# Kernel tuning notes

Measured on AMD Instinct MI355X. Metric: run time of the kernel, lower is better.

## Reference

```python
import jax, jax.numpy as jnp
import numpy as np

B, D, N = 2048, 512, 100000


def setup_inputs() -> dict:
    key = jax.random.key(0)
    k1, k2, k3 = jax.random.split(key, 3)
    queries = jax.random.normal(k1, (B, D), dtype=jnp.float32)
    X = jax.random.normal(k2, (N, D), dtype=jnp.float32)
    Y = jax.random.randint(k3, (N,), 0, 2, dtype=jnp.int64)
    return {"queries": queries, "X": X, "Y": Y, "K": 5}


def reference(queries, X, Y, K):
    # Pairwise squared Euclidean distance: ||q||^2 - 2 q.X^T + ||x||^2.
    # Use negative distance so lax.top_k returns nearest neighbors.
    q2 = jnp.sum(queries * queries, axis=1, keepdims=True)        # [B, 1]
    x2 = jnp.sum(X * X, axis=1)                                   # [N]
    neg_dist = 2.0 * (queries @ X.T) - q2 - x2[None, :]           # [B, N]
    _, idx = jax.lax.top_k(neg_dist, K)                           # [B, K]
    # Gather neighbor labels and count votes (fraction of class-1 neighbors).
    neighbor_labels = Y[idx].astype(jnp.float32)                  # [B, K]
    votes = jnp.mean(neighbor_labels, axis=1)                     # [B]
    # tf.pad(tf.expand_dims(votes, 1), [[0,0],[0,1]]) -> [B, 2]
    return jnp.pad(votes[:, None], ((0, 0), (0, 1)))
```

## Files before the change

### kernel.cpp

```cpp
#include <hip/hip_runtime.h>
#include <math.h>

typedef unsigned int   u32;
typedef unsigned short u16;
typedef short short8 __attribute__((ext_vector_type(8)));
typedef float f32x4  __attribute__((ext_vector_type(4)));

constexpr int B    = 2048;
constexpr int D    = 512;
constexpr int N    = 100000;
constexpr int KTOP = 5;
constexpr int NK   = 16;

constexpr int NPART    = 32;
constexpr int CHUNK    = 3136;
constexpr int PGPART   = CHUNK / 16;
constexpr int NPTS_PAD = NPART * CHUNK;
constexpr int NPG      = NPTS_PAD / 16;

__device__ __forceinline__ u16 f2bf(float f) {
    u32 u = __float_as_uint(f);
    return (u16)((u + 0x7fffu + ((u >> 16) & 1u)) >> 16);
}

__device__ __forceinline__ void gld_lds16(const void* g, void* l) {
    __builtin_amdgcn_global_load_lds((const __attribute__((address_space(1))) u32*)g,
                                     (__attribute__((address_space(3))) u32*)l, 16, 0, 0);
}

__device__ __forceinline__ void ins5(float (&s)[KTOP], int (&x)[KTOP], float v, int p) {
    if (v > s[KTOP - 1]) {
        s[KTOP - 1] = v; x[KTOP - 1] = p;
#pragma unroll
        for (int k = KTOP - 1; k > 0; --k) {
            if (s[k] > s[k - 1]) {
                float tf = s[k]; s[k] = s[k - 1]; s[k - 1] = tf;
                int   tg = x[k]; x[k] = x[k - 1]; x[k - 1] = tg;
            }
        }
    }
}

__device__ __forceinline__ void merge_xor(float (&s)[KTOP], int (&x)[KTOP], int mask) {
    float bs[KTOP], as[KTOP]; int bx[KTOP], ax[KTOP];
#pragma unroll
    for (int k = 0; k < KTOP; ++k) {
        bs[k] = __shfl_xor(s[k], mask); bx[k] = __shfl_xor(x[k], mask);
        as[k] = s[k]; ax[k] = x[k];
    }
#pragma unroll
    for (int k = 0; k < KTOP; ++k) {
        bool ta = (as[0] > bs[0]) || ((as[0] == bs[0]) && (ax[0] < bx[0]));
        s[k] = ta ? as[0] : bs[0];
        x[k] = ta ? ax[0] : bx[0];
#pragma unroll
        for (int m = 0; m < KTOP - 1; ++m) {
            as[m] = ta ? as[m + 1] : as[m];     ax[m] = ta ? ax[m + 1] : ax[m];
            bs[m] = ta ? bs[m]     : bs[m + 1]; bx[m] = ta ? bx[m]     : bx[m + 1];
        }
        as[KTOP - 1] = ta ? -INFINITY : as[KTOP - 1];
        bs[KTOP - 1] = ta ? bs[KTOP - 1] : -INFINITY;
    }
}

__global__ void prep_q(const float* __restrict__ Q, u16* __restrict__ Qbf) {
    int tid  = blockIdx.x * 256 + threadIdx.x;
    int q    = tid >> 6;
    int koct = tid & 63;
    const float4* src = (const float4*)(Q + (size_t)q * D + koct * 8);
    float4 a = src[0], b = src[1];
    u32 p0 = (u32)f2bf(a.x) | ((u32)f2bf(a.y) << 16);
    u32 p1 = (u32)f2bf(a.z) | ((u32)f2bf(a.w) << 16);
    u32 p2 = (u32)f2bf(b.x) | ((u32)f2bf(b.y) << 16);
    u32 p3 = (u32)f2bf(b.z) | ((u32)f2bf(b.w) << 16);
    int frag = (q >> 4) * NK + (koct >> 2);
    int lane = (q & 15) + 16 * (koct & 3);
    *(uint4*)(Qbf + (size_t)frag * 512 + lane * 8) = make_uint4(p0, p1, p2, p3);
}

__global__ void prep_x2(const float* __restrict__ X, u16* __restrict__ Xbf,
                        float* __restrict__ x2) {
    __shared__ float psum[4][16];
    const int t = threadIdx.x, lane = t & 63, wave = t >> 6;
    const int pg    = blockIdx.x;
    const int point = pg * 16 + (lane & 15);
    float ssum = 0.f;
#pragma unroll
    for (int u = 0; u < 4; ++u) {
        int k0i = wave * 4 + u;
        int k   = k0i * 32 + ((lane >> 4) << 3);
        uint4 o = make_uint4(0u, 0u, 0u, 0u);
        if (point < N) {
            const float4* src = (const float4*)(X + (size_t)point * D + k);
            float4 a = src[0], b = src[1];
            ssum = fmaf(a.x, a.x, ssum); ssum = fmaf(a.y, a.y, ssum);
            ssum = fmaf(a.z, a.z, ssum); ssum = fmaf(a.w, a.w, ssum);
            ssum = fmaf(b.x, b.x, ssum); ssum = fmaf(b.y, b.y, ssum);
            ssum = fmaf(b.z, b.z, ssum); ssum = fmaf(b.w, b.w, ssum);
            o.x = (u32)f2bf(a.x) | ((u32)f2bf(a.y) << 16);
            o.y = (u32)f2bf(a.z) | ((u32)f2bf(a.w) << 16);
            o.z = (u32)f2bf(b.x) | ((u32)f2bf(b.y) << 16);
            o.w = (u32)f2bf(b.z) | ((u32)f2bf(b.w) << 16);
        }
        *(uint4*)(Xbf + ((size_t)pg * 16 + k0i) * 512 + lane * 8) = o;
    }
    ssum += __shfl_xor(ssum, 16);
    ssum += __shfl_xor(ssum, 32);
    if (lane < 16) psum[wave][lane] = ssum;
    __syncthreads();
    if (t < 16) {
        float s = psum[0][t] + psum[1][t] + psum[2][t] + psum[3][t];
        x2[pg * 16 + t] = (pg * 16 + t < N) ? s : INFINITY;
    }
}

__global__ void x2_kernel(const float* __restrict__ X, float* __restrict__ x2, int total) {
    int lane = threadIdx.x & 63;
    int wid  = (int)((blockIdx.x * blockDim.x + threadIdx.x) >> 6);
    if (wid >= total) return;
    if (wid >= N) { if (lane == 0) x2[wid] = INFINITY; return; }
    const float* row = X + (size_t)wid * D;
    float s = 0.f;
    for (int c = lane; c < D; c += 64) { float v = row[c]; s = fmaf(v, v, s); }
#pragma unroll
    for (int off = 32; off > 0; off >>= 1) s += __shfl_down(s, off);
    if (lane == 0) x2[wid] = s;
}

__launch_bounds__(256, 2)
__global__ void knn_qreg(const u16* __restrict__ Xbf, const u16* __restrict__ Qbf,
                         const float* __restrict__ x2g,
                         float* __restrict__ cand_s, int* __restrict__ cand_i) {
    __shared__ __attribute__((aligned(16))) u16 Afr[2][16 * 512];
    const int t    = threadIdx.x;
    const int lane = t & 63;
    const int wave = t >> 6;
    const int quad = lane >> 4;
    const int col  = lane & 15;
    const int qb   = blockIdx.x;
    const int part = blockIdx.y;
    const int pg0    = part * PGPART;
    const int pstart = part * CHUNK;

    short8 bq[2][16];
#pragma unroll
    for (int j = 0; j < 2; ++j) {
        int qg = qb * 8 + wave * 2 + j;
#pragma unroll
        for (int k0i = 0; k0i < 16; ++k0i)
            bq[j][k0i] = *(const short8*)(Qbf + ((size_t)qg * 16 + k0i) * 512 + lane * 8);
    }

    float ss[2][KTOP]; int si[2][KTOP];
#pragma unroll
    for (int j = 0; j < 2; ++j)
#pragma unroll
        for (int k = 0; k < KTOP; ++k) { ss[j][k] = -INFINITY; si[j][k] = 0x7fffffff; }

    auto issue = [&](int pgi, int bsel) {
        const u16* src = Xbf + ((size_t)(pg0 + pgi) * 16 + wave * 4) * 512 + lane * 8;
        u16* dst = Afr[bsel] + (wave * 4) * 512;
#pragma unroll
        for (int f = 0; f < 4; ++f)
            gld_lds16(src + f * 512, dst + f * 512);
    };

    issue(0, 0);
    for (int pgi = 0; pgi < PGPART; ++pgi) {
        const int bsel = pgi & 1;
        __syncthreads();
        if (pgi + 1 < PGPART) issue(pgi + 1, bsel ^ 1);
        const int P = pstart + pgi * 16;
        float4 xx = *(const float4*)(x2g + P + quad * 4);

        f32x4 acc0 = (f32x4)0.f, acc1 = (f32x4)0.f;
#pragma unroll
        for (int k0i = 0; k0i < 16; ++k0i) {
            short8 af = *(const short8*)&Afr[bsel][k0i * 512 + lane * 8];
            acc0 = __builtin_amdgcn_mfma_f32_16x16x32_bf16(af, bq[0][k0i], acc0, 0, 0, 0);
            acc1 = __builtin_amdgcn_mfma_f32_16x16x32_bf16(af, bq[1][k0i], acc1, 0, 0, 0);
        }
        const int gbase = P + quad * 4;
        {
            float s0 = fmaf(2.f, acc0[0], -xx.x);
            float s1 = fmaf(2.f, acc0[1], -xx.y);
            float s2 = fmaf(2.f, acc0[2], -xx.z);
            float s3 = fmaf(2.f, acc0[3], -xx.w);
            float mx = fmaxf(fmaxf(s0, s1), fmaxf(s2, s3));
            if (mx > ss[0][KTOP - 1]) {
                ins5(ss[0], si[0], s0, gbase + 0);
                ins5(ss[0], si[0], s1, gbase + 1);
                ins5(ss[0], si[0], s2, gbase + 2);
                ins5(ss[0], si[0], s3, gbase + 3);
            }
        }
        {
            float s0 = fmaf(2.f, acc1[0], -xx.x);
            float s1 = fmaf(2.f, acc1[1], -xx.y);
            float s2 = fmaf(2.f, acc1[2], -xx.z);
            float s3 = fmaf(2.f, acc1[3], -xx.w);
            float mx = fmaxf(fmaxf(s0, s1), fmaxf(s2, s3));
            if (mx > ss[1][KTOP - 1]) {
                ins5(ss[1], si[1], s0, gbase + 0);
                ins5(ss[1], si[1], s1, gbase + 1);
                ins5(ss[1], si[1], s2, gbase + 2);
                ins5(ss[1], si[1], s3, gbase + 3);
            }
        }
    }

#pragma unroll
    for (int j = 0; j < 2; ++j) { merge_xor(ss[j], si[j], 16); merge_xor(ss[j], si[j], 32); }
    if (quad == 0) {
#pragma unroll
        for (int j = 0; j < 2; ++j) {
            int q = qb * 128 + wave * 32 + j * 16 + col;
            size_t base = ((size_t)q * NPART + part) * KTOP;
#pragma unroll
            for (int k = 0; k < KTOP; ++k) { cand_s[base + k] = ss[j][k]; cand_i[base + k] = si[j][k]; }
        }
    }
}

__launch_bounds__(256)
__global__ void knn_conv(const float* __restrict__ X, const u16* __restrict__ Qbf,
                         const float* __restrict__ x2g,
                         float* __restrict__ cand_s, int* __restrict__ cand_i) {
    __shared__ __attribute__((aligned(16))) u16 Bfr[16 * 512];
    __shared__ __attribute__((aligned(16))) u16 Afr[4 * 512];
    __shared__ float x2s[64];
    const int t = threadIdx.x, lane = t & 63, wave = t >> 6;
    const int quad = lane >> 4, col = lane & 15;
    const int qb = blockIdx.x, part = blockIdx.y;
    const int pstart = part * 782;
    const int pend   = min(pstart + 782, N);

    float ss[4][KTOP]; int si[4][KTOP];
#pragma unroll
    for (int j = 0; j < 4; ++j)
#pragma unroll
        for (int k = 0; k < KTOP; ++k) { ss[j][k] = -INFINITY; si[j][k] = 0x7fffffff; }

    const int nsub = (pend - pstart + 63) / 64;
    for (int sbi = 0; sbi < nsub; ++sbi) {
        const int sb = pstart + sbi * 64;
        __syncthreads();
        if (t < 64) x2s[t] = (sb + t < pend) ? x2g[sb + t] : INFINITY;
        f32x4 acc[4][4];
#pragma unroll
        for (int i = 0; i < 4; ++i)
#pragma unroll
            for (int j = 0; j < 4; ++j) acc[i][j] = (f32x4)0.f;
        for (int k0i = 0; k0i < NK; ++k0i) {
            const int k0 = k0i * 32;
            __syncthreads();
            {
                int prow = sb + wave * 16 + col;
                if (prow >= pend) prow = pend - 1;
                const float4* src = (const float4*)(X + (size_t)prow * D + k0 + quad * 8);
                float4 a = src[0], b = src[1];
                u32 p0 = (u32)f2bf(a.x) | ((u32)f2bf(a.y) << 16);
                u32 p1 = (u32)f2bf(a.z) | ((u32)f2bf(a.w) << 16);
                u32 p2 = (u32)f2bf(b.x) | ((u32)f2bf(b.y) << 16);
                u32 p3 = (u32)f2bf(b.z) | ((u32)f2bf(b.w) << 16);
                *(uint4*)(Afr + wave * 512 + lane * 8) = make_uint4(p0, p1, p2, p3);
            }
#pragma unroll
            for (int j = 0; j < 4; ++j) {
                int qgrp = qb * 16 + wave * 4 + j;
                gld_lds16(Qbf + ((size_t)qgrp * NK + k0i) * 512 + lane * 8,
                          (void*)(Bfr + (wave * 4 + j) * 512));
            }
            __syncthreads();
            short8 af[4], bqf[4];
#pragma unroll
            for (int i = 0; i < 4; ++i) af[i] = *(const short8*)(Afr + i * 512 + lane * 8);
#pragma unroll
            for (int j = 0; j < 4; ++j) bqf[j] = *(const short8*)(Bfr + (wave * 4 + j) * 512 + lane * 8);
#pragma unroll
            for (int i = 0; i < 4; ++i)
#pragma unroll
                for (int j = 0; j < 4; ++j)
                    acc[i][j] = __builtin_amdgcn_mfma_f32_16x16x32_bf16(af[i], bqf[j], acc[i][j], 0, 0, 0);
        }
#pragma unroll
        for (int i = 0; i < 4; ++i) {
            int pb = 16 * i + quad * 4;
#pragma unroll
            for (int j = 0; j < 4; ++j)
#pragma unroll
                for (int r = 0; r < 4; ++r)
                    ins5(ss[j], si[j], 2.f * acc[i][j][r] - x2s[pb + r], sb + pb + r);
        }
    }
#pragma unroll
    for (int j = 0; j < 4; ++j) { merge_xor(ss[j], si[j], 16); merge_xor(ss[j], si[j], 32); }
    if (quad == 0) {
#pragma unroll
        for (int j = 0; j < 4; ++j) {
            int qg = qb * 256 + wave * 64 + j * 16 + col;
            size_t base = ((size_t)qg * 128 + part) * KTOP;
#pragma unroll
            for (int k = 0; k < KTOP; ++k) { cand_s[base + k] = ss[j][k]; cand_i[base + k] = si[j][k]; }
        }
    }
}

__launch_bounds__(256)
__global__ void finalize(const float* __restrict__ Q, const float* __restrict__ X,
                         const float* __restrict__ x2g, const int* __restrict__ Y,
                         const float* __restrict__ cand_s, const int* __restrict__ cand_i,
                         float* __restrict__ out, int npart) {
    __shared__ float scs[4][96];
    __shared__ int   sis[4][96];
    const int t = threadIdx.x, lane = t & 63, w = t >> 6;
    const int q = blockIdx.x * 4 + w;
    const int perlane = npart * KTOP / 16;

    if (lane < 16) {
        float ls[KTOP]; int li[KTOP];
#pragma unroll
        for (int k = 0; k < KTOP; ++k) { ls[k] = -INFINITY; li[k] = 0x7fffffff; }
        const float* cs = cand_s + (size_t)q * npart * KTOP + lane * perlane;
        const int*   ci = cand_i + (size_t)q * npart * KTOP + lane * perlane;
        for (int c = 0; c < perlane; ++c) {
            float s = cs[c]; int p = ci[c];
            if (s > ls[KTOP - 1] || (s == ls[KTOP - 1] && p < li[KTOP - 1])) {
                ls[KTOP - 1] = s; li[KTOP - 1] = p;
#pragma unroll
                for (int k = KTOP - 1; k > 0; --k) {
                    bool up = (ls[k] > ls[k - 1]) || (ls[k] == ls[k - 1] && li[k] < li[k - 1]);
                    if (up) {
                        float tf = ls[k]; ls[k] = ls[k - 1]; ls[k - 1] = tf;
                        int   tg = li[k]; li[k] = li[k - 1]; li[k - 1] = tg;
                    }
                }
            }
        }
#pragma unroll
        for (int k = 0; k < KTOP; ++k) { scs[w][lane * KTOP + k] = ls[k]; sis[w][lane * KTOP + k] = li[k]; }
    }
    __syncthreads();
    if (lane == 0) {
        float bs[16]; int bx[16];
#pragma unroll
        for (int m = 0; m < 16; ++m) { bs[m] = -INFINITY; bx[m] = 0x7fffffff; }
        for (int c = 0; c < 80; ++c) {
            float s = scs[w][c]; int p = sis[w][c];
            if (s > bs[15] || (s == bs[15] && p < bx[15])) {
                bs[15] = s; bx[15] = p;
#pragma unroll
                for (int m = 15; m > 0; --m) {
                    bool up = (bs[m] > bs[m - 1]) || (bs[m] == bs[m - 1] && bx[m] < bx[m - 1]);
                    if (up) {
                        float tf = bs[m]; bs[m] = bs[m - 1]; bs[m - 1] = tf;
                        int   tg = bx[m]; bx[m] = bx[m - 1]; bx[m - 1] = tg;
                    }
                }
            }
        }
#pragma unroll
        for (int m = 0; m < 16; ++m) sis[w][80 + m] = bx[m];
    }
    __syncthreads();
    const int c = lane & 15, seg = lane >> 4;
    int idx = sis[w][80 + c];
    const float4* xr = (const float4*)(X + (size_t)idx * D);
    const float4* qr = (const float4*)(Q + (size_t)q * D);
    float d = 0.f;
    for (int u = seg * 32; u < seg * 32 + 32; ++u) {
        float4 a = qr[u], b = xr[u];
        d = fmaf(a.x, b.x, d); d = fmaf(a.y, b.y, d);
        d = fmaf(a.z, b.z, d); d = fmaf(a.w, b.w, d);
    }
    d += __shfl_xor(d, 16);
    d += __shfl_xor(d, 32);
    float sc = 2.f * d - x2g[idx];
    if (seg == 0) scs[w][80 + c] = sc;
    __syncthreads();
    if (lane == 0) {
        float bs[KTOP]; int bx[KTOP];
#pragma unroll
        for (int k = 0; k < KTOP; ++k) { bs[k] = -INFINITY; bx[k] = 0x7fffffff; }
        for (int c2 = 0; c2 < 16; ++c2) {
            float s = scs[w][80 + c2]; int p = sis[w][80 + c2];
            if (s > bs[KTOP - 1] || (s == bs[KTOP - 1] && p < bx[KTOP - 1])) {
                bs[KTOP - 1] = s; bx[KTOP - 1] = p;
#pragma unroll
                for (int k = KTOP - 1; k > 0; --k) {
                    bool up = (bs[k] > bs[k - 1]) || (bs[k] == bs[k - 1] && bx[k] < bx[k - 1]);
                    if (up) {
                        float tf = bs[k]; bs[k] = bs[k - 1]; bs[k - 1] = tf;
                        int   tg = bx[k]; bx[k] = bx[k - 1]; bx[k - 1] = tg;
                    }
                }
            }
        }
        float sum = 0.f;
#pragma unroll
        for (int k = 0; k < KTOP; ++k) sum += (float)Y[bx[k]];
        out[2 * q]     = sum * 0.2f;
        out[2 * q + 1] = 0.f;
    }
}

extern "C" void kernel_launch(void* const* d_in, const int* in_sizes, int n_in,
                              void* d_out, int out_size, void* d_ws, size_t ws_size,
                              hipStream_t stream) {
    const float* Qf = (const float*)d_in[0];
    const float* Xf = (const float*)d_in[1];
    const int*   Y  = (const int*)d_in[2];
    float* out = (float*)d_out;
    char* ws = (char*)d_ws;

    constexpr size_t XBF_B  = (size_t)NPG * NK * 1024;
    constexpr size_t QBF_B  = 2097152;
    constexpr size_t X2_B   = (size_t)NPTS_PAD * 4;
    constexpr size_t CAND_B = (size_t)B * NPART * KTOP * 4;
    constexpr size_t NEED   = XBF_B + QBF_B + X2_B + 2 * CAND_B;

    if (ws_size >= NEED) {
        u16*   Xbf    = (u16*)ws;
        u16*   Qbf    = (u16*)(ws + XBF_B);
        float* x2     = (float*)(ws + XBF_B + QBF_B);
        float* cand_s = (float*)(ws + XBF_B + QBF_B + X2_B);
        int*   cand_i = (int*)  (ws + XBF_B + QBF_B + X2_B + CAND_B);
        hipLaunchKernelGGL(prep_q,   dim3(512),           dim3(256), 0, stream, Qf, Qbf);
        hipLaunchKernelGGL(prep_x2,  dim3(NPG),           dim3(256), 0, stream, Xf, Xbf, x2);
        hipLaunchKernelGGL(knn_qreg, dim3(16, NPART),     dim3(256), 0, stream, Xbf, Qbf, x2, cand_s, cand_i);
        hipLaunchKernelGGL(finalize, dim3(B / 4),         dim3(256), 0, stream, Qf, Xf, x2, Y, cand_s, cand_i, out, NPART);
    } else {
        u16*   Qbf    = (u16*)ws;
        float* x2     = (float*)(ws + 2097152);
        float* cand_s = (float*)(ws + 2497152);
        int*   cand_i = (int*)  (ws + 7740032);
        hipLaunchKernelGGL(prep_q,    dim3(512),      dim3(256), 0, stream, Qf, Qbf);
        hipLaunchKernelGGL(x2_kernel, dim3(N / 4),    dim3(256), 0, stream, Xf, x2, N);
        hipLaunchKernelGGL(knn_conv,  dim3(8, 128),   dim3(256), 0, stream, Xf, Qbf, x2, cand_s, cand_i);
        hipLaunchKernelGGL(finalize,  dim3(B / 4),    dim3(256), 0, stream, Qf, Xf, x2, Y, cand_s, cand_i, out, 128);
    }
}
```

Measured before the change: 699.5 us.

## Double partitions, process two point groups per stage, swap grid axes

Raises the number of point partitions from 32 to 64 so the knn grid grows from 512 to 1024 blocks. Each pipeline stage now loads and computes two 16-point groups, giving four independent MFMA chains per step and halving the barrier count. The grid axes are swapped so adjacent blocks share the same query tile, and a compiler barrier keeps the query register loads in place. The costs are twice the LDS per block, more registers for accumulators, and twice as many candidates for finalize to merge.

New measurement: 692.7 us. Within noise of the previous version (-1.0%).

```diff
diff --git a/kernel.cpp b/kernel.cpp
--- a/kernel.cpp
+++ b/kernel.cpp
@@ -12,11 +12,12 @@
 constexpr int KTOP = 5;
 constexpr int NK   = 16;
 
-constexpr int NPART    = 32;
-constexpr int CHUNK    = 3136;
+constexpr int NPART    = 64;
+constexpr int CHUNK    = 1568;
 constexpr int PGPART   = CHUNK / 16;
 constexpr int NPTS_PAD = NPART * CHUNK;
 constexpr int NPG      = NPTS_PAD / 16;
+constexpr int ITERS    = PGPART / 2;
 
 __device__ __forceinline__ u16 f2bf(float f) {
     u32 u = __float_as_uint(f);
@@ -131,14 +132,14 @@
 __global__ void knn_qreg(const u16* __restrict__ Xbf, const u16* __restrict__ Qbf,
                          const float* __restrict__ x2g,
                          float* __restrict__ cand_s, int* __restrict__ cand_i) {
-    __shared__ __attribute__((aligned(16))) u16 Afr[2][16 * 512];
+    __shared__ __attribute__((aligned(16))) u16 Afr[2][32 * 512];
     const int t    = threadIdx.x;
     const int lane = t & 63;
     const int wave = t >> 6;
     const int quad = lane >> 4;
     const int col  = lane & 15;
-    const int qb   = blockIdx.x;
-    const int part = blockIdx.y;
+    const int part = blockIdx.x;
+    const int qb   = blockIdx.y;
     const int pg0    = part * PGPART;
     const int pstart = part * CHUNK;
 
@@ -150,6 +151,7 @@
         for (int k0i = 0; k0i < 16; ++k0i)
             bq[j][k0i] = *(const short8*)(Qbf + ((size_t)qg * 16 + k0i) * 512 + lane * 8);
     }
+    asm volatile("" ::: "memory");
 
     float ss[2][KTOP]; int si[2][KTOP];
 #pragma unroll
@@ -157,54 +159,79 @@
 #pragma unroll
         for (int k = 0; k < KTOP; ++k) { ss[j][k] = -INFINITY; si[j][k] = 0x7fffffff; }
 
-    auto issue = [&](int pgi, int bsel) {
-        const u16* src = Xbf + ((size_t)(pg0 + pgi) * 16 + wave * 4) * 512 + lane * 8;
-        u16* dst = Afr[bsel] + (wave * 4) * 512;
-#pragma unroll
-        for (int f = 0; f < 4; ++f)
-            gld_lds16(src + f * 512, dst + f * 512);
+    auto issue = [&](int it, int bsel) {
+        const size_t pgA = (size_t)(pg0 + 2 * it);
+        const u16* srcA = Xbf + (pgA * 16 + wave * 4) * 512 + (lane << 3);
+        u16* dstA = Afr[bsel] + (wave * 4) * 512;
+        u16* dstB = dstA + 16 * 512;
+#pragma unroll
+        for (int f = 0; f < 4; ++f) {
+            gld_lds16(srcA + f * 512, dstA + f * 512);
+            gld_lds16(srcA + (16 + f) * 512, dstB + f * 512);
+        }
     };
 
     issue(0, 0);
-    for (int pgi = 0; pgi < PGPART; ++pgi) {
-        const int bsel = pgi & 1;
+    for (int it = 0; it < ITERS; ++it) {
+        const int bsel = it & 1;
         __syncthreads();
-        if (pgi + 1 < PGPART) issue(pgi + 1, bsel ^ 1);
-        const int P = pstart + pgi * 16;
-        float4 xx = *(const float4*)(x2g + P + quad * 4);
-
-        f32x4 acc0 = (f32x4)0.f, acc1 = (f32x4)0.f;
+        if (it + 1 < ITERS) issue(it + 1, bsel ^ 1);
+        const int PA = pstart + (2 * it) * 16;
+        const int PB = PA + 16;
+        float4 xxA = *(const float4*)(x2g + PA + quad * 4);
+        float4 xxB = *(const float4*)(x2g + PB + quad * 4);
+
+        f32x4 accA0 = (f32x4)0.f, accA1 = (f32x4)0.f;
+        f32x4 accB0 = (f32x4)0.f, accB1 = (f32x4)0.f;
 #pragma unroll
         for (int k0i = 0; k0i < 16; ++k0i) {
-            short8 af = *(const short8*)&Afr[bsel][k0i * 512 + lane * 8];
-            acc0 = __builtin_amdgcn_mfma_f32_16x16x32_bf16(af, bq[0][k0i], acc0, 0, 0, 0);
-            acc1 = __builtin_amdgcn_mfma_f32_16x16x32_bf16(af, bq[1][k0i], acc1, 0, 0, 0);
-        }
-        const int gbase = P + quad * 4;
+            short8 afA = *(const short8*)&Afr[bsel][k0i * 512 + lane * 8];
+            short8 afB = *(const short8*)&Afr[bsel][(16 + k0i) * 512 + lane * 8];
+            accA0 = __builtin_amdgcn_mfma_f32_16x16x32_bf16(afA, bq[0][k0i], accA0, 0, 0, 0);
+            accA1 = __builtin_amdgcn_mfma_f32_16x16x32_bf16(afA, bq[1][k0i], accA1, 0, 0, 0);
+            accB0 = __builtin_amdgcn_mfma_f32_16x16x32_bf16(afB, bq[0][k0i], accB0, 0, 0, 0);
+            accB1 = __builtin_amdgcn_mfma_f32_16x16x32_bf16(afB, bq[1][k0i], accB1, 0, 0, 0);
+        }
         {
-            float s0 = fmaf(2.f, acc0[0], -xx.x);
-            float s1 = fmaf(2.f, acc0[1], -xx.y);
-            float s2 = fmaf(2.f, acc0[2], -xx.z);
-            float s3 = fmaf(2.f, acc0[3], -xx.w);
+            const int gbase = PA + quad * 4;
+            float s0 = fmaf(2.f, accA0[0], -xxA.x);
+            float s1 = fmaf(2.f, accA0[1], -xxA.y);
+            float s2 = fmaf(2.f, accA0[2], -xxA.z);
+            float s3 = fmaf(2.f, accA0[3], -xxA.w);
             float mx = fmaxf(fmaxf(s0, s1), fmaxf(s2, s3));
             if (mx > ss[0][KTOP - 1]) {
-                ins5(ss[0], si[0], s0, gbase + 0);
-                ins5(ss[0], si[0], s1, gbase + 1);
-                ins5(ss[0], si[0], s2, gbase + 2);
-                ins5(ss[0], si[0], s3, gbase + 3);
+                ins5(ss[0], si[0], s0, gbase + 0); ins5(ss[0], si[0], s1, gbase + 1);
+                ins5(ss[0], si[0], s2, gbase + 2); ins5(ss[0], si[0], s3, gbase + 3);
+            }
+            s0 = fmaf(2.f, accA1[0], -xxA.x);
+            s1 = fmaf(2.f, accA1[1], -xxA.y);
+            s2 = fmaf(2.f, accA1[2], -xxA.z);
+            s3 = fmaf(2.f, accA1[3], -xxA.w);
+            mx = fmaxf(fmaxf(s0, s1), fmaxf(s2, s3));
+            if (mx > ss[1][KTOP - 1]) {
+                ins5(ss[1], si[1], s0, gbase + 0); ins5(ss[1], si[1], s1, gbase + 1);
+                ins5(ss[1], si[1], s2, gbase + 2); ins5(ss[1], si[1], s3, gbase + 3);
             }
         }
         {
-            float s0 = fmaf(2.f, acc1[0], -xx.x);
-            float s1 = fmaf(2.f, acc1[1], -xx.y);
-            float s2 = fmaf(2.f, acc1[2], -xx.z);
-            float s3 = fmaf(2.f, acc1[3], -xx.w);
+            const int gbase = PB + quad * 4;
+            float s0 = fmaf(2.f, accB0[0], -xxB.x);
+            float s1 = fmaf(2.f, accB0[1], -xxB.y);
+            float s2 = fmaf(2.f, accB0[2], -xxB.z);
+            float s3 = fmaf(2.f, accB0[3], -xxB.w);
             float mx = fmaxf(fmaxf(s0, s1), fmaxf(s2, s3));
+            if (mx > ss[0][KTOP - 1]) {
+                ins5(ss[0], si[0], s0, gbase + 0); ins5(ss[0], si[0], s1, gbase + 1);
+                ins5(ss[0], si[0], s2, gbase + 2); ins5(ss[0], si[0], s3, gbase + 3);
+            }
+            s0 = fmaf(2.f, accB1[0], -xxB.x);
+            s1 = fmaf(2.f, accB1[1], -xxB.y);
+            s2 = fmaf(2.f, accB1[2], -xxB.z);
+            s3 = fmaf(2.f, accB1[3], -xxB.w);
+            mx = fmaxf(fmaxf(s0, s1), fmaxf(s2, s3));
             if (mx > ss[1][KTOP - 1]) {
-                ins5(ss[1], si[1], s0, gbase + 0);
-                ins5(ss[1], si[1], s1, gbase + 1);
-                ins5(ss[1], si[1], s2, gbase + 2);
-                ins5(ss[1], si[1], s3, gbase + 3);
+                ins5(ss[1], si[1], s0, gbase + 0); ins5(ss[1], si[1], s1, gbase + 1);
+                ins5(ss[1], si[1], s2, gbase + 2); ins5(ss[1], si[1], s3, gbase + 3);
             }
         }
     }
@@ -425,10 +452,10 @@
         float* x2     = (float*)(ws + XBF_B + QBF_B);
         float* cand_s = (float*)(ws + XBF_B + QBF_B + X2_B);
         int*   cand_i = (int*)  (ws + XBF_B + QBF_B + X2_B + CAND_B);
-        hipLaunchKernelGGL(prep_q,   dim3(512),           dim3(256), 0, stream, Qf, Qbf);
-        hipLaunchKernelGGL(prep_x2,  dim3(NPG),           dim3(256), 0, stream, Xf, Xbf, x2);
-        hipLaunchKernelGGL(knn_qreg, dim3(16, NPART),     dim3(256), 0, stream, Xbf, Qbf, x2, cand_s, cand_i);
-        hipLaunchKernelGGL(finalize, dim3(B / 4),         dim3(256), 0, stream, Qf, Xf, x2, Y, cand_s, cand_i, out, NPART);
+        hipLaunchKernelGGL(prep_q,   dim3(512),       dim3(256), 0, stream, Qf, Qbf);
+        hipLaunchKernelGGL(prep_x2,  dim3(NPG),       dim3(256), 0, stream, Xf, Xbf, x2);
+        hipLaunchKernelGGL(knn_qreg, dim3(NPART, 16), dim3(256), 0, stream, Xbf, Qbf, x2, cand_s, cand_i);
+        hipLaunchKernelGGL(finalize, dim3(B / 4),     dim3(256), 0, stream, Qf, Xf, x2, Y, cand_s, cand_i, out, NPART);
     } else {
         u16*   Qbf    = (u16*)ws;
         float* x2     = (float*)(ws + 2097152);
```
